# Optimization experiments

Measured on AMD Instinct MI355X. Metric: run time of the kernel, lower is better.

## Reference

```python
import jax, jax.numpy as jnp
import numpy as np

N = 100000   # nodes
E = 600000   # edges per sign
IN = 128     # in_dim
HID = 128    # hidden_dim
H = 8        # num_heads
D = HID // H # per-head out_feats = 16
OUT = 64     # out_dim
NEG_SLOPE = 0.2


def setup_inputs() -> dict:
    key = jax.random.key(0)
    ks = jax.random.split(key, 20)
    inp = {}
    inp['features'] = jax.random.normal(ks[0], (N, IN), dtype=jnp.float32)
    inp['pos_src'] = jax.random.randint(ks[1], (E,), 0, N, dtype=jnp.int32)
    inp['pos_dst'] = jax.random.randint(ks[2], (E,), 0, N, dtype=jnp.int32)
    inp['neg_src'] = jax.random.randint(ks[3], (E,), 0, N, dtype=jnp.int32)
    inp['neg_dst'] = jax.random.randint(ks[4], (E,), 0, N, dtype=jnp.int32)
    # GATConv params (DGL: fc weight, attn_l, attn_r, bias) for pos and neg convs
    s = 0.1
    inp['W_pos'] = jax.random.normal(ks[5], (IN, H * D), dtype=jnp.float32) * s
    inp['al_pos'] = jax.random.normal(ks[6], (H, D), dtype=jnp.float32) * s
    inp['ar_pos'] = jax.random.normal(ks[7], (H, D), dtype=jnp.float32) * s
    inp['b_pos'] = jnp.zeros((H * D,), dtype=jnp.float32)
    inp['W_neg'] = jax.random.normal(ks[8], (IN, H * D), dtype=jnp.float32) * s
    inp['al_neg'] = jax.random.normal(ks[9], (H, D), dtype=jnp.float32) * s
    inp['ar_neg'] = jax.random.normal(ks[10], (H, D), dtype=jnp.float32) * s
    inp['b_neg'] = jnp.zeros((H * D,), dtype=jnp.float32)
    # final MLP: Linear(2*HID, HID) -> ReLU -> Linear(HID, OUT)
    inp['W1'] = jax.random.normal(ks[11], (2 * HID, HID), dtype=jnp.float32) * s
    inp['b1'] = jnp.zeros((HID,), dtype=jnp.float32)
    inp['W2'] = jax.random.normal(ks[12], (HID, OUT), dtype=jnp.float32) * s
    inp['b2'] = jnp.zeros((OUT,), dtype=jnp.float32)
    return inp


def gat_conv(features, src, dst, W, al, ar, b, n):
    # DGL GATConv (eval mode, no feat/attn dropout, no residual/activation)
    feat = (features @ W).reshape(n, H, D)            # [N,H,D]
    el = (feat * al).sum(-1)                          # [N,H]
    er = (feat * ar).sum(-1)                          # [N,H]
    e = jax.nn.leaky_relu(el[src] + er[dst], NEG_SLOPE)  # [E,H] per-edge logits
    # edge softmax over incoming edges of each dst node, per head
    m = jax.ops.segment_max(e, dst, num_segments=n)   # [N,H]
    ex = jnp.exp(e - m[dst])                          # [E,H]
    s = jax.ops.segment_sum(ex, dst, num_segments=n)  # [N,H]
    a = ex / s[dst]                                   # [E,H]
    rst = jax.ops.segment_sum(a[:, :, None] * feat[src], dst, num_segments=n)  # [N,H,D]
    return rst.reshape(n, H * D) + b


def reference(features, pos_src, pos_dst, neg_src, neg_dst,
              W_pos, al_pos, ar_pos, b_pos,
              W_neg, al_neg, ar_neg, b_neg,
              W1, b1, W2, b2):
    n = features.shape[0]
    h_pos = gat_conv(features, pos_src, pos_dst, W_pos, al_pos, ar_pos, b_pos, n)
    h_neg = gat_conv(features, neg_src, neg_dst, W_neg, al_neg, ar_neg, b_neg, n)
    h = jnp.concatenate([h_pos, h_neg], axis=1)       # [N, 2*HID]
    h_final = jnp.maximum(h @ W1 + b1, 0.0) @ W2 + b2  # [N, OUT]
    return (h_pos, h_neg, h_final)
```

## Files before the change

### kernel.cpp

```cpp
#include <hip/hip_runtime.h>

#define NEG_SLOPE 0.2f

typedef __attribute__((ext_vector_type(8))) short short8;
typedef __attribute__((ext_vector_type(4))) float floatx4;

__device__ __forceinline__ unsigned short f2bf(float f) {
    union { float f; unsigned u; } v; v.f = f;
    unsigned r = v.u + 0x7FFF + ((v.u >> 16) & 1);
    return (unsigned short)(r >> 16);
}
__device__ __forceinline__ float bf2f(unsigned short u) {
    return __uint_as_float(((unsigned)u) << 16);
}

__global__ void convert_w_kernel(const float* __restrict__ Wp, const float* __restrict__ Wn,
                                 const float* __restrict__ W1, const float* __restrict__ W2,
                                 unsigned short* __restrict__ Wcat, unsigned short* __restrict__ W1t,
                                 unsigned short* __restrict__ W2t) {
    int i = blockIdx.x * blockDim.x + threadIdx.x;
    if (i < 256 * 128) {
        int nr = i >> 7, k = i & 127;
        float v = (nr < 128) ? Wp[k * 128 + nr] : Wn[k * 128 + (nr - 128)];
        Wcat[i] = f2bf(v);
    } else if (i < 256 * 128 + 128 * 256) {
        int j = i - 256 * 128;
        int nr = j >> 8, k = j & 255;
        W1t[j] = f2bf(W1[k * 128 + nr]);
    } else if (i < 256 * 128 + 128 * 256 + 64 * 128) {
        int j = i - 256 * 128 - 128 * 256;
        int nr = j >> 7, k = j & 127;
        W2t[j] = f2bf(W2[k * 64 + nr]);
    }
}

template<int KDIM, int N, bool IN_F32, bool RELU, bool OUT_BF16, bool SPLIT>
__global__ __launch_bounds__(256)
void gemm_stream_kernel(const void* __restrict__ Av, const unsigned short* __restrict__ Wt,
                        const float* __restrict__ bias, void* __restrict__ outv, int n_rows) {
    constexpr int KS = KDIM / 32;
    constexpr int NT = N / 16;
    static_assert(N * KDIM * 2 <= 65536, "LDS budget");
    __shared__ __align__(16) unsigned short Bs[N * KDIM];
    const int tid = threadIdx.x;

    constexpr int CH = (N * KDIM) / 8;
    for (int i = tid; i < CH; i += 256) {
        int r = i / (KDIM / 8), c8 = i % (KDIM / 8);
        float4 v = *(const float4*)(Wt + (size_t)r * KDIM + c8 * 8);
        unsigned byt = ((unsigned)(r * KDIM + c8 * 8) << 1) ^ ((unsigned)(r & 7) << 4);
        *(float4*)((char*)Bs + byt) = v;
    }
    __syncthreads();

    const int lane = tid & 63;
    const int lrow = lane & 15;
    const int q = lane >> 4;
    const unsigned swz = (unsigned)(lrow & 7) << 4;
    const char* const Bsb = (const char*)Bs + lrow * (2 * KDIM);
    const int gw = blockIdx.x * 4 + (tid >> 6);
    const int nw = gridDim.x * 4;
    const int ntiles = n_rows >> 4;

    for (int t = gw; t < ntiles; t += nw) {
        const int arow = t * 16 + lrow;
        short8 af[KS];
        if (IN_F32) {
            const float* Af = (const float*)Av + (size_t)arow * KDIM + q * 8;
#pragma unroll
            for (int ks = 0; ks < KS; ++ks) {
                float4 va = *(const float4*)(Af + ks * 32);
                float4 vb = *(const float4*)(Af + ks * 32 + 4);
                unsigned short o[8];
                o[0] = f2bf(va.x); o[1] = f2bf(va.y); o[2] = f2bf(va.z); o[3] = f2bf(va.w);
                o[4] = f2bf(vb.x); o[5] = f2bf(vb.y); o[6] = f2bf(vb.z); o[7] = f2bf(vb.w);
                af[ks] = *(short8*)o;
            }
        } else {
            const unsigned short* Ab = (const unsigned short*)Av + (size_t)arow * KDIM + q * 8;
#pragma unroll
            for (int ks = 0; ks < KS; ++ks)
                af[ks] = *(const short8*)(Ab + ks * 32);
        }

        floatx4 acc[NT];
#pragma unroll
        for (int nt = 0; nt < NT; ++nt) acc[nt] = (floatx4){0.f, 0.f, 0.f, 0.f};

#pragma unroll
        for (int ks = 0; ks < KS; ++ks) {
            const char* bp = Bsb + (((unsigned)(ks * 64 + q * 16)) ^ swz);
#pragma unroll
            for (int nt = 0; nt < NT; ++nt) {
                short8 bf = *(const short8*)(bp + nt * (16 * 2 * KDIM));
                acc[nt] = __builtin_amdgcn_mfma_f32_16x16x32_bf16(af[ks], bf, acc[nt], 0, 0, 0);
            }
        }

#pragma unroll
        for (int nt = 0; nt < NT; ++nt) {
            const int cl = nt * 16 + lrow;
            const float bv = bias ? bias[cl] : 0.f;
#pragma unroll
            for (int r = 0; r < 4; ++r) {
                const int grow = t * 16 + q * 4 + r;
                float v = acc[nt][r] + bv;
                if (RELU) v = fmaxf(v, 0.f);
                if (SPLIT) {
                    unsigned short* op = (unsigned short*)outv +
                        ((nt >= NT / 2) ? (size_t)n_rows * (N / 2) : (size_t)0);
                    op[(size_t)grow * (N / 2) + (cl & (N / 2 - 1))] = f2bf(v);
                } else if (OUT_BF16) {
                    ((unsigned short*)outv)[(size_t)grow * N + cl] = f2bf(v);
                } else {
                    ((float*)outv)[(size_t)grow * N + cl] = v;
                }
            }
        }
    }
}

__global__ void eler_kernel(const unsigned short* __restrict__ featb,
                            const float* __restrict__ al_p, const float* __restrict__ ar_p,
                            const float* __restrict__ al_n, const float* __restrict__ ar_n,
                            float* __restrict__ el_p, float* __restrict__ er_p,
                            float* __restrict__ el_n, float* __restrict__ er_n, int n) {
    int idx = blockIdx.x * blockDim.x + threadIdx.x;
    if (idx >= 2 * n * 8) return;
    int h = idx & 7;
    bool neg = idx >= n * 8;
    const float* al = neg ? al_n : al_p;
    const float* ar = neg ? ar_n : ar_p;
    float* el = neg ? el_n : el_p;
    float* er = neg ? er_n : er_p;
    int local = neg ? idx - n * 8 : idx;
    const unsigned* fu = (const unsigned*)(featb + (size_t)idx * 16);
    float sl = 0.f, sr = 0.f;
#pragma unroll
    for (int q = 0; q < 8; ++q) {
        unsigned u = fu[q];
        float lo = __uint_as_float(u << 16);
        float hi = __uint_as_float(u & 0xFFFF0000u);
        sl += lo * al[h * 16 + q * 2] + hi * al[h * 16 + q * 2 + 1];
        sr += lo * ar[h * 16 + q * 2] + hi * ar[h * 16 + q * 2 + 1];
    }
    el[local] = sl; er[local] = sr;
}

__global__ void count_kernel(const int* __restrict__ pos_dst, const int* __restrict__ neg_dst,
                             int* __restrict__ cnt, int ne, int npad) {
    int e = blockIdx.x * blockDim.x + threadIdx.x;
    if (e < ne) atomicAdd(&cnt[pos_dst[e]], 1);
    else if (e < 2 * ne) atomicAdd(&cnt[npad + neg_dst[e - ne]], 1);
}

__global__ __launch_bounds__(256)
void scan1_kernel(int* __restrict__ cnt, int* __restrict__ bsum) {
    __shared__ int sm[256];
    int i = blockIdx.x * 256 + threadIdx.x;
    int v = cnt[i];
    sm[threadIdx.x] = v;
    __syncthreads();
    for (int off = 1; off < 256; off <<= 1) {
        int t = (threadIdx.x >= off) ? sm[threadIdx.x - off] : 0;
        __syncthreads();
        sm[threadIdx.x] += t;
        __syncthreads();
    }
    cnt[i] = sm[threadIdx.x] - v;
    if (threadIdx.x == 255) bsum[blockIdx.x] = sm[255];
}

__global__ __launch_bounds__(512)
void scan2_kernel(int* __restrict__ bsum, int nb) {
    __shared__ int sm[512];
    int base = blockIdx.x * nb;
    int v = (threadIdx.x < nb) ? bsum[base + threadIdx.x] : 0;
    sm[threadIdx.x] = v;
    __syncthreads();
    for (int off = 1; off < 512; off <<= 1) {
        int t = (threadIdx.x >= off) ? sm[threadIdx.x - off] : 0;
        __syncthreads();
        sm[threadIdx.x] += t;
        __syncthreads();
    }
    if (threadIdx.x < nb) bsum[base + threadIdx.x] = sm[threadIdx.x] - v;
}

__global__ void scan3_kernel(int* __restrict__ cnt, const int* __restrict__ bsum,
                             int* __restrict__ offs_p, int* __restrict__ offs_n,
                             int n, int ne, int npad) {
    int i = blockIdx.x * blockDim.x + threadIdx.x;
    int v = cnt[i] + bsum[i >> 8];
    cnt[i] = v;
    if (i < n) offs_p[i] = v;
    else if (i >= npad && i - npad < n) offs_n[i - npad] = v;
    if (i == 0) { offs_p[n] = ne; offs_n[n] = ne; }
}

__global__ void scatter_kernel(const int* __restrict__ pos_src, const int* __restrict__ pos_dst,
                               const int* __restrict__ neg_src, const int* __restrict__ neg_dst,
                               int* __restrict__ cur, int* __restrict__ ssrc_p, int* __restrict__ ssrc_n,
                               int ne, int npad) {
    int e = blockIdx.x * blockDim.x + threadIdx.x;
    if (e < ne) {
        int p = atomicAdd(&cur[pos_dst[e]], 1);
        ssrc_p[p] = pos_src[e];
    } else if (e < 2 * ne) {
        int j = e - ne;
        int p = atomicAdd(&cur[npad + neg_dst[j]], 1);
        ssrc_n[p] = neg_src[j];
    }
}

__global__ __launch_bounds__(256)
void gat_gather_kernel(const int* __restrict__ offs_p, const int* __restrict__ offs_n,
                       const int* __restrict__ ssrc_p, const int* __restrict__ ssrc_n,
                       const float* __restrict__ el_p, const float* __restrict__ er_p,
                       const float* __restrict__ el_n, const float* __restrict__ er_n,
                       const unsigned short* __restrict__ featb,
                       const float* __restrict__ b_pos, const float* __restrict__ b_neg,
                       float* __restrict__ out, unsigned short* __restrict__ hcatb, int n) {
    int node = (blockIdx.x * 256 + threadIdx.x) >> 6;
    int lane = threadIdx.x & 63;
    if (node >= n) return;
    const int neg = blockIdx.y;
    const int* offs = neg ? offs_n : offs_p;
    const int* ssrc = neg ? ssrc_n : ssrc_p;
    const float* el = neg ? el_n : el_p;
    const float* er = neg ? er_n : er_p;
    const unsigned short* fb = featb + (size_t)(neg ? n : 0) * 128;
    const float* bias = neg ? b_neg : b_pos;
    float* o = out + (size_t)(neg ? n : 0) * 128;
    const int coloff = neg ? 128 : 0;

    const int h = lane >> 3;
    const float erh = er[(size_t)node * 8 + h];
    const int beg = offs[node], end = offs[node + 1];
    float acc0 = 0.f, acc1 = 0.f, denom = 0.f;

#define GSTEP(S)  do {                                                         \
        float x_ = el[(size_t)(S) * 8 + h] + erh;                              \
        x_ = x_ < 0.f ? NEG_SLOPE * x_ : x_;                                   \
        float w_ = __expf(x_);                                                 \
        denom += w_;                                                           \
        ushort2 f_ = *(const ushort2*)(fb + (size_t)(S) * 128 + lane * 2);     \
        acc0 = fmaf(w_, bf2f(f_.x), acc0);                                     \
        acc1 = fmaf(w_, bf2f(f_.y), acc1);                                     \
    } while (0)

    for (int p0 = beg; p0 < end; p0 += 64) {
        int cnt = end - p0; if (cnt > 64) cnt = 64;
        int sid = (lane < cnt) ? ssrc[p0 + lane] : 0;
        int j = 0;
        for (; j + 4 <= cnt; j += 4) {
            int s0 = __shfl(sid, j), s1 = __shfl(sid, j + 1);
            int s2 = __shfl(sid, j + 2), s3 = __shfl(sid, j + 3);
            GSTEP(s0); GSTEP(s1); GSTEP(s2); GSTEP(s3);
        }
        for (; j < cnt; ++j) {
            int s = __shfl(sid, j);
            GSTEP(s);
        }
    }
#undef GSTEP

    float inv = denom > 0.f ? 1.f / denom : 0.f;
    float2 ov;
    ov.x = fmaf(acc0, inv, bias[lane * 2]);
    ov.y = fmaf(acc1, inv, bias[lane * 2 + 1]);
    *(float2*)(o + (size_t)node * 128 + lane * 2) = ov;
    ushort2 hb; hb.x = f2bf(ov.x); hb.y = f2bf(ov.y);
    *(ushort2*)(hcatb + (size_t)node * 256 + coloff + lane * 2) = hb;
}

extern "C" void kernel_launch(void* const* d_in, const int* in_sizes, int n_in,
                              void* d_out, int out_size, void* d_ws, size_t ws_size,
                              hipStream_t stream) {
    const float* features = (const float*)d_in[0];
    const int* pos_src = (const int*)d_in[1];
    const int* pos_dst = (const int*)d_in[2];
    const int* neg_src = (const int*)d_in[3];
    const int* neg_dst = (const int*)d_in[4];
    const float* W_pos  = (const float*)d_in[5];
    const float* al_pos = (const float*)d_in[6];
    const float* ar_pos = (const float*)d_in[7];
    const float* b_pos  = (const float*)d_in[8];
    const float* W_neg  = (const float*)d_in[9];
    const float* al_neg = (const float*)d_in[10];
    const float* ar_neg = (const float*)d_in[11];
    const float* b_neg  = (const float*)d_in[12];
    const float* W1 = (const float*)d_in[13];
    const float* b1 = (const float*)d_in[14];
    const float* W2 = (const float*)d_in[15];
    const float* b2 = (const float*)d_in[16];

    const int n  = in_sizes[0] / 128;
    const int ne = in_sizes[1];
    const int nb = (n + 255) / 256;
    const int npad = nb * 256;

    float* out  = (float*)d_out;
    float* hfin = out + (size_t)n * 256;

    unsigned short* featb = (unsigned short*)d_ws;
    unsigned short* hcatb = featb + (size_t)2 * n * 128;
    unsigned short* mid   = hcatb + (size_t)n * 256;
    float* el_pos = (float*)(mid + (size_t)n * 128);
    float* er_pos = el_pos + (size_t)n * 8;
    float* el_neg = er_pos + (size_t)n * 8;
    float* er_neg = el_neg + (size_t)n * 8;
    unsigned short* Wcat = (unsigned short*)(er_neg + (size_t)n * 8);
    unsigned short* W1t  = Wcat + 256 * 128;
    unsigned short* W2t  = W1t + 128 * 256;
    int* cnt      = (int*)(W2t + 64 * 128);
    int* offs_pos = cnt + 2 * npad;
    int* offs_neg = offs_pos + (n + 1);
    int* bsum     = offs_neg + (n + 1);
    int* ssrc_pos = bsum + 2 * nb;
    int* ssrc_neg = ssrc_pos + ne;

    const int ge2 = (2 * ne + 255) / 256;

    convert_w_kernel<<<(73728 + 255) / 256, 256, 0, stream>>>(W_pos, W_neg, W1, W2, Wcat, W1t, W2t);

    hipMemsetAsync(cnt, 0, sizeof(int) * 2 * (size_t)npad, stream);
    count_kernel<<<ge2, 256, 0, stream>>>(pos_dst, neg_dst, cnt, ne, npad);
    scan1_kernel<<<2 * nb, 256, 0, stream>>>(cnt, bsum);
    scan2_kernel<<<2, 512, 0, stream>>>(bsum, nb);
    scan3_kernel<<<2 * nb, 256, 0, stream>>>(cnt, bsum, offs_pos, offs_neg, n, ne, npad);
    scatter_kernel<<<ge2, 256, 0, stream>>>(pos_src, pos_dst, neg_src, neg_dst, cnt, ssrc_pos, ssrc_neg, ne, npad);

    gemm_stream_kernel<128, 256, true, false, true, true>
        <<<512, 256, 0, stream>>>(features, Wcat, nullptr, featb, n);

    eler_kernel<<<(2 * n * 8 + 255) / 256, 256, 0, stream>>>(featb, al_pos, ar_pos, al_neg, ar_neg,
                                                             el_pos, er_pos, el_neg, er_neg, n);

    gat_gather_kernel<<<dim3((n + 3) / 4, 2), 256, 0, stream>>>(offs_pos, offs_neg, ssrc_pos, ssrc_neg,
                                                                el_pos, er_pos, el_neg, er_neg,
                                                                featb, b_pos, b_neg, out, hcatb, n);

    gemm_stream_kernel<256, 128, false, true, true, false>
        <<<512, 256, 0, stream>>>(hcatb, W1t, b1, mid, n);
    gemm_stream_kernel<128, 64, false, false, false, false>
        <<<512, 256, 0, stream>>>(mid, W2t, b2, hfin, n);
}
```

Baseline: 535.6 us.

## Fuse the two MLP GEMMs into one kernel reading fp32 GAT outputs

Replaces the two separate MLP GEMM launches with one fused kernel. It keeps W1 and W2 in LDS, converts the fp32 h_pos/h_neg outputs to bf16 on the fly, and passes the ReLU intermediate through per-wave LDS scratch. The gather kernel no longer writes a separate bf16 concatenated copy, and its output store becomes nontemporal. This removes the hcatb and mid global round trips and one launch, at the cost of reading fp32 activations (twice the bytes) and lower occupancy from the large LDS footprint.

Result: slower. 578.7 us (+8.0%).

```diff
diff --git a/kernel.cpp b/kernel.cpp
--- a/kernel.cpp
+++ b/kernel.cpp
@@ -4,6 +4,7 @@
 
 typedef __attribute__((ext_vector_type(8))) short short8;
 typedef __attribute__((ext_vector_type(4))) float floatx4;
+typedef __attribute__((ext_vector_type(2))) float floatx2;
 
 __device__ __forceinline__ unsigned short f2bf(float f) {
     union { float f; unsigned u; } v; v.f = f;
@@ -120,6 +121,115 @@
     }
 }
 
+__global__ __launch_bounds__(512)
+void mlp_fused_kernel(const float* __restrict__ outp,
+                      const unsigned short* __restrict__ W1t, const unsigned short* __restrict__ W2t,
+                      const float* __restrict__ b1, const float* __restrict__ b2,
+                      float* __restrict__ hfin, int n_rows) {
+    constexpr int K1 = 256, N1 = 128, KS1 = 8, NT1 = 8;
+    constexpr int K2 = 128, N2 = 64, KS2 = 4, NT2 = 4;
+    __shared__ __align__(16) unsigned short Bs1[N1 * K1];
+    __shared__ __align__(16) unsigned short Bs2[N2 * K2];
+    __shared__ __align__(16) unsigned short scr[8 * 16 * 128];
+    const int tid = threadIdx.x;
+
+    for (int i = tid; i < N1 * K1 / 8; i += 512) {
+        int r = i >> 5, c8 = i & 31;
+        float4 v = *(const float4*)(W1t + (size_t)r * K1 + c8 * 8);
+        unsigned byt = ((unsigned)(r * K1 + c8 * 8) << 1) ^ ((unsigned)(r & 7) << 4);
+        *(float4*)((char*)Bs1 + byt) = v;
+    }
+    for (int i = tid; i < N2 * K2 / 8; i += 512) {
+        int r = i >> 4, c8 = i & 15;
+        float4 v = *(const float4*)(W2t + (size_t)r * K2 + c8 * 8);
+        unsigned byt = ((unsigned)(r * K2 + c8 * 8) << 1) ^ ((unsigned)(r & 7) << 4);
+        *(float4*)((char*)Bs2 + byt) = v;
+    }
+    __syncthreads();
+
+    const int lane = tid & 63;
+    const int wave = tid >> 6;
+    const int lrow = lane & 15;
+    const int q = lane >> 4;
+    const unsigned swz = (unsigned)(lrow & 7) << 4;
+    const char* const B1b = (const char*)Bs1 + lrow * (2 * K1);
+    const char* const B2b = (const char*)Bs2 + lrow * (2 * K2);
+    char* const scw = (char*)scr + wave * 4096;
+    const int gw = blockIdx.x * 8 + wave;
+    const int nw = gridDim.x * 8;
+    const int ntiles = n_rows >> 4;
+
+    for (int t = gw; t < ntiles; t += nw) {
+        const int arow = t * 16 + lrow;
+        const float* Ap = outp + (size_t)arow * 128 + q * 8;
+        const float* An = outp + (size_t)(n_rows + arow) * 128 + q * 8;
+        short8 af[KS1];
+#pragma unroll
+        for (int ks = 0; ks < KS1; ++ks) {
+            const float* src = (ks < 4) ? (Ap + ks * 32) : (An + (ks - 4) * 32);
+            float4 va = *(const float4*)(src);
+            float4 vb = *(const float4*)(src + 4);
+            unsigned short o[8];
+            o[0] = f2bf(va.x); o[1] = f2bf(va.y); o[2] = f2bf(va.z); o[3] = f2bf(va.w);
+            o[4] = f2bf(vb.x); o[5] = f2bf(vb.y); o[6] = f2bf(vb.z); o[7] = f2bf(vb.w);
+            af[ks] = *(short8*)o;
+        }
+
+        floatx4 acc1[NT1];
+#pragma unroll
+        for (int nt = 0; nt < NT1; ++nt) acc1[nt] = (floatx4){0.f, 0.f, 0.f, 0.f};
+#pragma unroll
+        for (int ks = 0; ks < KS1; ++ks) {
+            const char* bp = B1b + (((unsigned)(ks * 64 + q * 16)) ^ swz);
+#pragma unroll
+            for (int nt = 0; nt < NT1; ++nt) {
+                short8 bf = *(const short8*)(bp + nt * (16 * 2 * K1));
+                acc1[nt] = __builtin_amdgcn_mfma_f32_16x16x32_bf16(af[ks], bf, acc1[nt], 0, 0, 0);
+            }
+        }
+
+#pragma unroll
+        for (int nt = 0; nt < NT1; ++nt) {
+            const int cl = nt * 16 + lrow;
+            const float bv = b1[cl];
+#pragma unroll
+            for (int r = 0; r < 4; ++r) {
+                int row = q * 4 + r;
+                float v = fmaxf(acc1[nt][r] + bv, 0.f);
+                unsigned byt = ((unsigned)(row * 256 + cl * 2)) ^ ((unsigned)(row & 7) << 4);
+                *(unsigned short*)(scw + byt) = f2bf(v);
+            }
+        }
+        short8 af2[KS2];
+#pragma unroll
+        for (int ks = 0; ks < KS2; ++ks)
+            af2[ks] = *(const short8*)(scw + (((unsigned)(lrow * 256 + ks * 64 + q * 16)) ^ swz));
+
+        floatx4 acc2[NT2];
+#pragma unroll
+        for (int nt = 0; nt < NT2; ++nt) acc2[nt] = (floatx4){0.f, 0.f, 0.f, 0.f};
+#pragma unroll
+        for (int ks = 0; ks < KS2; ++ks) {
+            const char* bp = B2b + (((unsigned)(ks * 64 + q * 16)) ^ swz);
+#pragma unroll
+            for (int nt = 0; nt < NT2; ++nt) {
+                short8 bf = *(const short8*)(bp + nt * (16 * 2 * K2));
+                acc2[nt] = __builtin_amdgcn_mfma_f32_16x16x32_bf16(af2[ks], bf, acc2[nt], 0, 0, 0);
+            }
+        }
+#pragma unroll
+        for (int nt = 0; nt < NT2; ++nt) {
+            const int cl = nt * 16 + lrow;
+            const float bv = b2[cl];
+#pragma unroll
+            for (int r = 0; r < 4; ++r) {
+                const int grow = t * 16 + q * 4 + r;
+                __builtin_nontemporal_store(acc2[nt][r] + bv, hfin + (size_t)grow * 64 + cl);
+            }
+        }
+    }
+}
+
 __global__ void eler_kernel(const unsigned short* __restrict__ featb,
                             const float* __restrict__ al_p, const float* __restrict__ ar_p,
                             const float* __restrict__ al_n, const float* __restrict__ ar_n,
@@ -220,7 +330,7 @@
                        const float* __restrict__ el_n, const float* __restrict__ er_n,
                        const unsigned short* __restrict__ featb,
                        const float* __restrict__ b_pos, const float* __restrict__ b_neg,
-                       float* __restrict__ out, unsigned short* __restrict__ hcatb, int n) {
+                       float* __restrict__ out, int n) {
     int node = (blockIdx.x * 256 + threadIdx.x) >> 6;
     int lane = threadIdx.x & 63;
     if (node >= n) return;
@@ -232,7 +342,6 @@
     const unsigned short* fb = featb + (size_t)(neg ? n : 0) * 128;
     const float* bias = neg ? b_neg : b_pos;
     float* o = out + (size_t)(neg ? n : 0) * 128;
-    const int coloff = neg ? 128 : 0;
 
     const int h = lane >> 3;
     const float erh = er[(size_t)node * 8 + h];
@@ -266,12 +375,10 @@
 #undef GSTEP
 
     float inv = denom > 0.f ? 1.f / denom : 0.f;
-    float2 ov;
+    floatx2 ov;
     ov.x = fmaf(acc0, inv, bias[lane * 2]);
     ov.y = fmaf(acc1, inv, bias[lane * 2 + 1]);
-    *(float2*)(o + (size_t)node * 128 + lane * 2) = ov;
-    ushort2 hb; hb.x = f2bf(ov.x); hb.y = f2bf(ov.y);
-    *(ushort2*)(hcatb + (size_t)node * 256 + coloff + lane * 2) = hb;
+    __builtin_nontemporal_store(ov, (floatx2*)(o + (size_t)node * 128 + lane * 2));
 }
 
 extern "C" void kernel_launch(void* const* d_in, const int* in_sizes, int n_in,
@@ -304,9 +411,7 @@
     float* hfin = out + (size_t)n * 256;
 
     unsigned short* featb = (unsigned short*)d_ws;
-    unsigned short* hcatb = featb + (size_t)2 * n * 128;
-    unsigned short* mid   = hcatb + (size_t)n * 256;
-    float* el_pos = (float*)(mid + (size_t)n * 128);
+    float* el_pos = (float*)(featb + (size_t)2 * n * 128);
     float* er_pos = el_pos + (size_t)n * 8;
     float* el_neg = er_pos + (size_t)n * 8;
     float* er_neg = el_neg + (size_t)n * 8;
@@ -339,10 +444,7 @@
 
     gat_gather_kernel<<<dim3((n + 3) / 4, 2), 256, 0, stream>>>(offs_pos, offs_neg, ssrc_pos, ssrc_neg,
                                                                 el_pos, er_pos, el_neg, er_neg,
-                                                                featb, b_pos, b_neg, out, hcatb, n);
-
-    gemm_stream_kernel<256, 128, false, true, true, false>
-        <<<512, 256, 0, stream>>>(hcatb, W1t, b1, mid, n);
-    gemm_stream_kernel<128, 64, false, false, false, false>
-        <<<512, 256, 0, stream>>>(mid, W2t, b2, hfin, n);
-}
+                                                                featb, b_pos, b_neg, out, n);
+
+    mlp_fused_kernel<<<256, 512, 0, stream>>>(out, W1t, W2t, b1, b2, hfin, n);
+}
```
